# Optimization experiments

Hardware: AMD Instinct MI355X
Metric: run time of the kernel (lower is better)

The kernel has to match this reference:

```python
import jax, jax.numpy as jnp
import numpy as np

HID, OUT, D = 256, 64, 128
N_ITEM, N_USER, E = 100000, 50000, 800000


def sage_conv(x_src, x_dst, src, dst, w_l, b_l, w_r, n_dst):
    # PyG SAGEConv (mean aggr): out = lin_l(mean_j x_src[j]) + lin_r(x_dst)
    msg = x_src[src]                                        # [E, d_src] gather
    agg = jax.ops.segment_sum(msg, dst, num_segments=n_dst)  # [n_dst, d_src]
    cnt = jax.ops.segment_sum(jnp.ones((src.shape[0],), x_src.dtype), dst,
                              num_segments=n_dst)
    mean = agg / jnp.clip(cnt, 1.0, None)[:, None]
    return mean @ w_l + b_l + x_dst @ w_r


def setup_inputs() -> dict:
    key = jax.random.key(0)
    ks = jax.random.split(key, 16)
    sc = lambda d: 1.0 / np.sqrt(d)
    inp = {
        "x_item": jax.random.normal(ks[0], (N_ITEM, D), jnp.float32),
        "x_user": jax.random.normal(ks[1], (N_USER, D), jnp.float32),
        "ei_ii_src": jax.random.randint(ks[2], (E,), 0, N_ITEM),
        "ei_ii_dst": jax.random.randint(ks[3], (E,), 0, N_ITEM),
        "ei_iu_src": jax.random.randint(ks[4], (E,), 0, N_ITEM),
        "ei_iu_dst": jax.random.randint(ks[5], (E,), 0, N_USER),
        # conv1: item->item, in (D, D) -> HID
        "w_l1": jax.random.normal(ks[6], (D, HID), jnp.float32) * sc(D),
        "b1": jnp.zeros((HID,), jnp.float32),
        "w_r1": jax.random.normal(ks[7], (D, HID), jnp.float32) * sc(D),
        # conv2: (item D, user D) -> HID
        "w_l2": jax.random.normal(ks[8], (D, HID), jnp.float32) * sc(D),
        "b2": jnp.zeros((HID,), jnp.float32),
        "w_r2": jax.random.normal(ks[9], (D, HID), jnp.float32) * sc(D),
        # conv3: (item HID, user HID) -> HID
        "w_l3": jax.random.normal(ks[10], (HID, HID), jnp.float32) * sc(HID),
        "b3": jnp.zeros((HID,), jnp.float32),
        "w_r3": jax.random.normal(ks[11], (HID, HID), jnp.float32) * sc(HID),
        # final linear HID -> OUT
        "w_lin": jax.random.normal(ks[12], (HID, OUT), jnp.float32) * sc(HID),
        "b_lin": jnp.zeros((OUT,), jnp.float32),
    }
    return inp


def reference(x_item, x_user, ei_ii_src, ei_ii_dst, ei_iu_src, ei_iu_dst,
              w_l1, b1, w_r1, w_l2, b2, w_r2, w_l3, b3, w_r3, w_lin, b_lin):
    item_x = jax.nn.relu(sage_conv(x_item, x_item, ei_ii_src, ei_ii_dst,
                                   w_l1, b1, w_r1, N_ITEM))
    user_x = jax.nn.relu(sage_conv(x_item, x_user, ei_iu_src, ei_iu_dst,
                                   w_l2, b2, w_r2, N_USER))
    user_x = jax.nn.relu(sage_conv(item_x, user_x, ei_iu_src, ei_iu_dst,
                                   w_l3, b3, w_r3, N_USER))
    return user_x @ w_lin + b_lin
```

## Files before the change

kernel.cpp:

```cpp
#include <hip/hip_runtime.h>
#include <hip/hip_bf16.h>

#define N_ITEM 100000
#define N_USER 50000
#define D_IN   128
#define HID    256
#define OUT_D  64
#define CAP    64

#define S1B   391
#define CV1B  1024
#define CV2B  512
#define PK1B  68
#define G1 (S1B + CV1B + CV2B + PK1B)

#define S2B   391
#define A1B   3125
#define G2 (S2B + A1B)

#define C1B   782
#define A2B   1563
#define G3 (C1B + A2B)

#define C2B   391
#define A3LB  1568
#define G4 (C2B + A3LB)

#define C3LB  196
#define A3HB  1557
#define G5 (C3LB + A3HB)

#define C3HB  195
#define FLB   196
#define G6 (C3HB + FLB)

#define FHB   195

typedef __attribute__((ext_vector_type(8))) short bf16x8;
typedef __attribute__((ext_vector_type(4))) float f32x4;

__device__ inline float b2f(unsigned int h) {
    union { unsigned int u; float f; } c; c.u = h << 16; return c.f;
}
__device__ inline unsigned short f2b(float f) {
    unsigned int u = __builtin_bit_cast(unsigned int, f);
    u += 0x7fff + ((u >> 16) & 1);
    return (unsigned short)(u >> 16);
}

__device__ __forceinline__ void scatter_body(
    const int* __restrict__ src, const int* __restrict__ dstl,
    int* __restrict__ cur, int* __restrict__ slot, int E, int t)
{
    int e4 = t * 4;
    if (e4 + 3 < E) {
        int4 d = *(const int4*)&dstl[e4];
        int4 s = *(const int4*)&src[e4];
        int p0 = atomicAdd(&cur[d.x], 1);
        int p1 = atomicAdd(&cur[d.y], 1);
        int p2 = atomicAdd(&cur[d.z], 1);
        int p3 = atomicAdd(&cur[d.w], 1);
        if (p0 < CAP) slot[d.x * CAP + p0] = s.x;
        if (p1 < CAP) slot[d.y * CAP + p1] = s.y;
        if (p2 < CAP) slot[d.z * CAP + p2] = s.z;
        if (p3 < CAP) slot[d.w * CAP + p3] = s.w;
    } else {
        for (int e = e4; e < E; ++e) {
            int d0 = dstl[e], s0 = src[e];
            int p = atomicAdd(&cur[d0], 1);
            if (p < CAP) slot[d0 * CAP + p] = s0;
        }
    }
}

__device__ __forceinline__ void agg_mean128_q(
    const unsigned short* __restrict__ xsrc,
    const int* __restrict__ sl, int num, int ql,
    unsigned short* __restrict__ dstrow)
{
    const unsigned short* xb = xsrc + ql * 8;
    float acc[8] = {};
    int j = 0;
    for (; j + 8 <= num; j += 8) {
        int s[8];
        #pragma unroll
        for (int u = 0; u < 8; ++u) s[u] = sl[j + u];
        uint4 v[8];
        #pragma unroll
        for (int u = 0; u < 8; ++u)
            v[u] = *(const uint4*)(xb + (size_t)s[u] * 256);
        #pragma unroll
        for (int u = 0; u < 8; ++u) {
            acc[0] += b2f(v[u].x & 0xffffu);
            acc[1] += b2f(v[u].x >> 16);
            acc[2] += b2f(v[u].y & 0xffffu);
            acc[3] += b2f(v[u].y >> 16);
            acc[4] += b2f(v[u].z & 0xffffu);
            acc[5] += b2f(v[u].z >> 16);
            acc[6] += b2f(v[u].w & 0xffffu);
            acc[7] += b2f(v[u].w >> 16);
        }
    }
    for (; j < num; ++j) {
        uint4 v = *(const uint4*)(xb + (size_t)sl[j] * 256);
        acc[0] += b2f(v.x & 0xffffu);
        acc[1] += b2f(v.x >> 16);
        acc[2] += b2f(v.y & 0xffffu);
        acc[3] += b2f(v.y >> 16);
        acc[4] += b2f(v.z & 0xffffu);
        acc[5] += b2f(v.z >> 16);
        acc[6] += b2f(v.w & 0xffffu);
        acc[7] += b2f(v.w >> 16);
    }
    float sc = 1.0f / fmaxf((float)num, 1.0f);
    uint4 w;
    w.x = (unsigned int)f2b(acc[0] * sc) | ((unsigned int)f2b(acc[1] * sc) << 16);
    w.y = (unsigned int)f2b(acc[2] * sc) | ((unsigned int)f2b(acc[3] * sc) << 16);
    w.z = (unsigned int)f2b(acc[4] * sc) | ((unsigned int)f2b(acc[5] * sc) << 16);
    w.w = (unsigned int)f2b(acc[6] * sc) | ((unsigned int)f2b(acc[7] * sc) << 16);
    *(uint4*)(dstrow + ql * 8) = w;
}

__device__ __forceinline__ void agg_mean256_body(
    const unsigned short* __restrict__ xsrc,
    const int* __restrict__ sl, int num, int hl,
    unsigned short* __restrict__ dstrow)
{
    const unsigned short* xb = xsrc + hl * 8;
    float acc[8] = {};
    int j = 0;
    for (; j + 8 <= num; j += 8) {
        int s[8];
        #pragma unroll
        for (int u = 0; u < 8; ++u) s[u] = sl[j + u];
        uint4 v[8];
        #pragma unroll
        for (int u = 0; u < 8; ++u)
            v[u] = *(const uint4*)(xb + (size_t)s[u] * 256);
        #pragma unroll
        for (int u = 0; u < 8; ++u) {
            acc[0] += b2f(v[u].x & 0xffffu);
            acc[1] += b2f(v[u].x >> 16);
            acc[2] += b2f(v[u].y & 0xffffu);
            acc[3] += b2f(v[u].y >> 16);
            acc[4] += b2f(v[u].z & 0xffffu);
            acc[5] += b2f(v[u].z >> 16);
            acc[6] += b2f(v[u].w & 0xffffu);
            acc[7] += b2f(v[u].w >> 16);
        }
    }
    for (; j < num; ++j) {
        uint4 v = *(const uint4*)(xb + (size_t)sl[j] * 256);
        acc[0] += b2f(v.x & 0xffffu);
        acc[1] += b2f(v.x >> 16);
        acc[2] += b2f(v.y & 0xffffu);
        acc[3] += b2f(v.y >> 16);
        acc[4] += b2f(v.z & 0xffffu);
        acc[5] += b2f(v.z >> 16);
        acc[6] += b2f(v.w & 0xffffu);
        acc[7] += b2f(v.w >> 16);
    }
    float sc = 1.0f / fmaxf((float)num, 1.0f);
    uint4 w;
    w.x = (unsigned int)f2b(acc[0] * sc) | ((unsigned int)f2b(acc[1] * sc) << 16);
    w.y = (unsigned int)f2b(acc[2] * sc) | ((unsigned int)f2b(acc[3] * sc) << 16);
    w.z = (unsigned int)f2b(acc[4] * sc) | ((unsigned int)f2b(acc[5] * sc) << 16);
    w.w = (unsigned int)f2b(acc[6] * sc) | ((unsigned int)f2b(acc[7] * sc) << 16);
    *(uint4*)(dstrow + hl * 8) = w;
}

__device__ inline void pack_unit(const float* __restrict__ wl,
                                 const float* __restrict__ wr,
                                 int K, int NCv, unsigned short* __restrict__ dst,
                                 int u)
{
    int kb = u / NCv, col = u - kb * NCv;
    int colp = col ^ (kb & 7);
    unsigned short tmp[8];
    #pragma unroll
    for (int j = 0; j < 8; ++j) {
        int k = kb * 8 + j;
        float w = (k < K) ? wl[(size_t)k * NCv + col]
                          : wr[(size_t)(k - K) * NCv + col];
        tmp[j] = f2b(w);
    }
    *(uint4*)&dst[((size_t)kb * NCv + colp) * 8] = *(const uint4*)tmp;
}

__global__ __launch_bounds__(512) void prep1_kernel(
    const int* __restrict__ ii_src, const int* __restrict__ ii_dst,
    int* __restrict__ cur_i, int* __restrict__ slot_ii, int E,
    const float* __restrict__ x_item, const float* __restrict__ x_user,
    unsigned short* __restrict__ Acat1, unsigned short* __restrict__ Acat2,
    const float* __restrict__ wl1, const float* __restrict__ wr1,
    const float* __restrict__ wl2, const float* __restrict__ wr2,
    const float* __restrict__ wl3, const float* __restrict__ wr3,
    const float* __restrict__ wlin,
    unsigned short* __restrict__ Wp1, unsigned short* __restrict__ Wp2,
    unsigned short* __restrict__ Wp3, unsigned short* __restrict__ Wpl)
{
    int b = blockIdx.x;
    if (b < S1B) {
        scatter_body(ii_src, ii_dst, cur_i, slot_ii, E, b * 512 + threadIdx.x);
    } else if (b < S1B + CV1B) {
        const int STR = CV1B * 512;
        for (int u = (b - S1B) * 512 + threadIdx.x; u < N_ITEM * 32; u += STR) {
            int row = u >> 5, c4 = (u & 31) * 4;
            float4 v = *(const float4*)&x_item[(size_t)row * 128 + c4];
            ushort4 o;
            o.x = f2b(v.x); o.y = f2b(v.y); o.z = f2b(v.z); o.w = f2b(v.w);
            *(ushort4*)&Acat1[(size_t)row * 256 + 128 + c4] = o;
        }
    } else if (b < S1B + CV1B + CV2B) {
        const int STR = CV2B * 512;
        for (int u = (b - S1B - CV1B) * 512 + threadIdx.x; u < N_USER * 32; u += STR) {
            int row = u >> 5, c4 = (u & 31) * 4;
            float4 v = *(const float4*)&x_user[(size_t)row * 128 + c4];
            ushort4 o;
            o.x = f2b(v.x); o.y = f2b(v.y); o.z = f2b(v.z); o.w = f2b(v.w);
            *(ushort4*)&Acat2[(size_t)row * 256 + 128 + c4] = o;
        }
    } else {
        int t = (b - S1B - CV1B - CV2B) * 512 + threadIdx.x;
        if (t < 8192)       pack_unit(wl1, wr1, 128, 256, Wp1, t);
        else if (t < 16384) pack_unit(wl2, wr2, 128, 256, Wp2, t - 8192);
        else if (t < 32768) pack_unit(wl3, wr3, 256, 256, Wp3, t - 16384);
        else if (t < 34816) pack_unit(wlin, wlin, 256, 64, Wpl, t - 32768);
    }
}

__global__ __launch_bounds__(512) void prep2_kernel(
    const int* __restrict__ iu_src, const int* __restrict__ iu_dst,
    int* __restrict__ cur_u, int* __restrict__ slot_iu, int E,
    const unsigned short* __restrict__ xsrc,
    const int* __restrict__ slot_ii, const int* __restrict__ cur_i,
    unsigned short* __restrict__ Acat1)
{
    int b = blockIdx.x;
    if (b < S2B) {
        scatter_body(iu_src, iu_dst, cur_u, slot_iu, E, b * 512 + threadIdx.x);
        return;
    }
    int row = (b - S2B) * 32 + (threadIdx.x >> 4);
    int ql = threadIdx.x & 15;
    const int* sl = slot_ii + (size_t)row * CAP;
    int num = min(cur_i[row], CAP);
    agg_mean128_q(xsrc, sl, num, ql, Acat1 + (size_t)row * 256);
}

template <int NC, int WM, int WN, bool OUT_BF16, bool RELU>
__device__ __forceinline__ void gemm_body(
    int bid,
    const unsigned short* __restrict__ A, int lda,
    const unsigned short* __restrict__ Wp,
    const float* __restrict__ bias,
    void* __restrict__ Cout, int ldc, int col_off,
    int nrows, int nkt)
{
    constexpr int BM = 128;
    constexpr int MR = WM / 16, NR = WN / 16;
    constexpr int NWC = NC / WN;
    __shared__ unsigned short As[BM * 64];
    __shared__ unsigned short Bs[64 * NC];

    const int tid  = threadIdx.x;
    const int wave = tid >> 6;
    const int lane = tid & 63;
    const int row0 = bid * BM;
    const int wr = wave / NWC;
    const int wc = wave % NWC;

    f32x4 acc[MR][NR];
    #pragma unroll
    for (int m = 0; m < MR; ++m)
        #pragma unroll
        for (int n = 0; n < NR; ++n)
            acc[m][n] = (f32x4){0.f, 0.f, 0.f, 0.f};

    for (int kt = 0; kt < nkt; ++kt) {
        #pragma unroll
        for (int c = 0; c < 2; ++c) {
            int i = wave * 2 + c;
            int rl = 8 * i + (lane >> 3);
            int kc = (lane & 7) ^ (lane >> 3);
            const unsigned short* g =
                A + (size_t)(row0 + rl) * lda + kt * 64 + kc * 8;
            __builtin_amdgcn_global_load_lds(
                (const __attribute__((address_space(1))) void*)g,
                (__attribute__((address_space(3))) void*)(As + i * 512), 16, 0, 0);
        }
        constexpr int BCALLS = (64 * NC * 2) / 1024;
        constexpr int PW = BCALLS / 8;
        #pragma unroll
        for (int c = 0; c < PW; ++c) {
            int j = wave * PW + c;
            const unsigned short* g =
                Wp + (size_t)kt * (8 * NC * 8) + (size_t)j * 512 + lane * 8;
            __builtin_amdgcn_global_load_lds(
                (const __attribute__((address_space(1))) void*)g,
                (__attribute__((address_space(3))) void*)(Bs + j * 512), 16, 0, 0);
        }
        __syncthreads();

        #pragma unroll
        for (int kk = 0; kk < 2; ++kk) {
            bf16x8 af[MR], bfr[NR];
            #pragma unroll
            for (int m = 0; m < MR; ++m) {
                int row = wr * WM + m * 16 + (lane & 15);
                int kc = ((kk * 4) + (lane >> 4)) ^ (lane & 7);
                af[m] = *(const bf16x8*)(As + row * 64 + kc * 8);
            }
            #pragma unroll
            for (int n = 0; n < NR; ++n) {
                int kb = kk * 4 + (lane >> 4);
                int col = (wc * WN + n * 16 + (lane & 15)) ^ (kb & 7);
                bfr[n] = *(const bf16x8*)(Bs + (kb * NC + col) * 8);
            }
            #pragma unroll
            for (int m = 0; m < MR; ++m)
                #pragma unroll
                for (int n = 0; n < NR; ++n)
                    acc[m][n] = __builtin_amdgcn_mfma_f32_16x16x32_bf16(
                        af[m], bfr[n], acc[m][n], 0, 0, 0);
        }
        __syncthreads();
    }

    #pragma unroll
    for (int n = 0; n < NR; ++n) {
        int col = wc * WN + n * 16 + (lane & 15);
        float bv = bias[col];
        #pragma unroll
        for (int m = 0; m < MR; ++m) {
            #pragma unroll
            for (int j = 0; j < 4; ++j) {
                int row = row0 + wr * WM + m * 16 + (lane >> 4) * 4 + j;
                if (row < nrows) {
                    float v = acc[m][n][j] + bv;
                    if (RELU) v = fmaxf(v, 0.f);
                    if (OUT_BF16)
                        ((unsigned short*)Cout)[(size_t)row * ldc + col_off + col] = f2b(v);
                    else
                        ((float*)Cout)[(size_t)row * ldc + col_off + col] = v;
                }
            }
        }
    }
}

template <int NC, int WM, int WN, bool OUT_BF16, bool RELU>
__global__ __launch_bounds__(512) void gemm_mfma(
    int bid_base,
    const unsigned short* __restrict__ A, int lda,
    const unsigned short* __restrict__ Wp,
    const float* __restrict__ bias,
    void* __restrict__ Cout, int ldc, int col_off,
    int nrows, int nkt)
{
    gemm_body<NC, WM, WN, OUT_BF16, RELU>(bid_base + blockIdx.x, A, lda, Wp,
                                          bias, Cout, ldc, col_off, nrows, nkt);
}

__global__ __launch_bounds__(512) void conv1_agg2_kernel(
    const unsigned short* __restrict__ Acat1,
    const unsigned short* __restrict__ Wp1,
    const float* __restrict__ b1,
    unsigned short* __restrict__ item_x,
    const unsigned short* __restrict__ xsrc,
    const int* __restrict__ slot_iu, const int* __restrict__ cur_u,
    unsigned short* __restrict__ Acat2)
{
    if (blockIdx.x < C1B) {
        gemm_body<256, 64, 64, true, true>(blockIdx.x, Acat1, 256, Wp1, b1,
                                           item_x, 256, 0, N_ITEM, 4);
        return;
    }
    int row = (blockIdx.x - C1B) * 32 + (threadIdx.x >> 4);
    if (row >= N_USER) return;
    int ql = threadIdx.x & 15;
    const int* sl = slot_iu + (size_t)row * CAP;
    int num = min(cur_u[row], CAP);
    agg_mean128_q(xsrc, sl, num, ql, Acat2 + (size_t)row * 256);
}

__global__ __launch_bounds__(512) void conv2_agg3_kernel(
    const unsigned short* __restrict__ Acat2,
    const unsigned short* __restrict__ Wp2,
    const float* __restrict__ b2,
    unsigned short* __restrict__ Acat3,
    const unsigned short* __restrict__ item_x,
    const int* __restrict__ slot_iu, const int* __restrict__ cur_u)
{
    if (blockIdx.x < C2B) {
        gemm_body<256, 64, 64, true, true>(blockIdx.x, Acat2, 256, Wp2, b2,
                                           Acat3, 512, 256, N_USER, 4);
        return;
    }
    int row = (blockIdx.x - C2B) * 16 + (threadIdx.x >> 5);
    int hl = threadIdx.x & 31;
    const int* sl = slot_iu + (size_t)row * CAP;
    int num = min(cur_u[row], CAP);
    agg_mean256_body(item_x, sl, num, hl, Acat3 + (size_t)row * 512);
}

__global__ __launch_bounds__(512) void conv3_agg3b_kernel(
    const unsigned short* __restrict__ Acat3r,
    unsigned short* __restrict__ Acat3w,
    const unsigned short* __restrict__ Wp3,
    const float* __restrict__ b3,
    unsigned short* __restrict__ ux3,
    const unsigned short* __restrict__ item_x,
    const int* __restrict__ slot_iu, const int* __restrict__ cur_u)
{
    if (blockIdx.x < C3LB) {
        gemm_body<256, 64, 64, true, true>(blockIdx.x, Acat3r, 512, Wp3, b3,
                                           ux3, 256, 0, N_USER, 8);
        return;
    }
    int row = 25088 + (blockIdx.x - C3LB) * 16 + (threadIdx.x >> 5);
    int hl = threadIdx.x & 31;
    const int* sl = slot_iu + (size_t)row * CAP;
    int num = min(cur_u[row], CAP);
    agg_mean256_body(item_x, sl, num, hl, Acat3w + (size_t)row * 512);
}

__global__ __launch_bounds__(512) void conv3b_final_kernel(
    const unsigned short* __restrict__ Acat3,
    const unsigned short* __restrict__ Wp3,
    const float* __restrict__ b3,
    unsigned short* __restrict__ ux3,
    const unsigned short* __restrict__ Wpl,
    const float* __restrict__ b_lin,
    float* __restrict__ out)
{
    if (blockIdx.x < C3HB) {
        gemm_body<256, 64, 64, true, true>(C3LB + blockIdx.x, Acat3, 512, Wp3,
                                           b3, ux3, 256, 0, N_USER, 8);
    } else {
        gemm_body<64, 16, 64, false, false>(blockIdx.x - C3HB, ux3, 256, Wpl,
                                            b_lin, out, 64, 0, N_USER, 4);
    }
}

extern "C" void kernel_launch(void* const* d_in, const int* in_sizes, int n_in,
                              void* d_out, int out_size, void* d_ws, size_t ws_size,
                              hipStream_t stream)
{
    const float* x_item = (const float*)d_in[0];
    const float* x_user = (const float*)d_in[1];
    const int* ii_src   = (const int*)d_in[2];
    const int* ii_dst   = (const int*)d_in[3];
    const int* iu_src   = (const int*)d_in[4];
    const int* iu_dst   = (const int*)d_in[5];
    const float* w_l1 = (const float*)d_in[6];
    const float* b1   = (const float*)d_in[7];
    const float* w_r1 = (const float*)d_in[8];
    const float* w_l2 = (const float*)d_in[9];
    const float* b2   = (const float*)d_in[10];
    const float* w_r2 = (const float*)d_in[11];
    const float* w_l3 = (const float*)d_in[12];
    const float* b3   = (const float*)d_in[13];
    const float* w_r3 = (const float*)d_in[14];
    const float* w_lin = (const float*)d_in[15];
    const float* b_lin = (const float*)d_in[16];
    float* out = (float*)d_out;

    const int E = in_sizes[2];
    const int NIP = 100096;
    const int NUP = 50048;

    int* cur_i   = (int*)d_ws;
    int* cur_u   = cur_i + 100352;
    int* slot_ii = cur_u + 50176;
    int* slot_iu = slot_ii + (size_t)N_ITEM * CAP;

    unsigned short* Acat1  = (unsigned short*)(slot_iu + (size_t)N_USER * CAP);
    unsigned short* item_x = Acat1  + (size_t)NIP * 256;
    unsigned short* Acat2  = item_x + (size_t)NIP * 256;
    unsigned short* Acat3  = Acat2  + (size_t)NUP * 256;
    unsigned short* ux3    = Acat3  + (size_t)NUP * 512;
    unsigned short* Wp1    = ux3    + (size_t)NUP * 256;
    unsigned short* Wp2    = Wp1 + 65536;
    unsigned short* Wp3    = Wp2 + 65536;
    unsigned short* Wpl    = Wp3 + 131072;

    hipMemsetAsync(cur_i, 0, (size_t)150528 * 4, stream);

    prep1_kernel<<<G1, 512, 0, stream>>>(
        ii_src, ii_dst, cur_i, slot_ii, E,
        x_item, x_user, Acat1, Acat2,
        w_l1, w_r1, w_l2, w_r2, w_l3, w_r3, w_lin,
        Wp1, Wp2, Wp3, Wpl);

    prep2_kernel<<<G2, 512, 0, stream>>>(
        iu_src, iu_dst, cur_u, slot_iu, E,
        Acat1 + 128, slot_ii, cur_i, Acat1);

    conv1_agg2_kernel<<<G3, 512, 0, stream>>>(
        Acat1, Wp1, b1, item_x,
        Acat1 + 128, slot_iu, cur_u, Acat2);

    conv2_agg3_kernel<<<G4, 512, 0, stream>>>(
        Acat2, Wp2, b2, Acat3, item_x, slot_iu, cur_u);

    conv3_agg3b_kernel<<<G5, 512, 0, stream>>>(
        Acat3, Acat3, Wp3, b3, ux3, item_x, slot_iu, cur_u);

    conv3b_final_kernel<<<G6, 512, 0, stream>>>(
        Acat3, Wp3, b3, ux3, Wpl, b_lin, out);

    gemm_mfma<64, 16, 64, false, false><<<FHB, 512, 0, stream>>>(
        FLB, ux3, 256, Wpl, b_lin, out, 64, 0, N_USER, 4);
}
```

Measured before the change: 370.2 us.

## Replace staggered conv3/final overlap kernels with full agg then plain GEMMs

Removes the split scheme where conv3's GEMM and the final linear layer were run in halves alongside the remaining aggregation work across three launches. Conv2_agg3 now aggregates all user rows in one pass, followed by two plain GEMM launches for conv3 and the final projection. This simplifies the schedule and drops one launch, but gives up the overlap of GEMM work with the memory-bound aggregation. Launch counts use NUP/128, whose definition is not shown.

After: 365.2 us. About the same (-1.3%).

```diff
diff --git a/kernel.cpp b/kernel.cpp
--- a/kernel.cpp
+++ b/kernel.cpp
@@ -23,18 +23,8 @@
 #define G3 (C1B + A2B)
 
 #define C2B   391
-#define A3LB  1568
-#define G4 (C2B + A3LB)
-
-#define C3LB  196
-#define A3HB  1557
-#define G5 (C3LB + A3HB)
-
-#define C3HB  195
-#define FLB   196
-#define G6 (C3HB + FLB)
-
-#define FHB   195
+#define A3B   3125
+#define G4 (C2B + A3B)
 
 typedef __attribute__((ext_vector_type(8))) short bf16x8;
 typedef __attribute__((ext_vector_type(4))) float f32x4;
@@ -351,14 +341,13 @@
 
 template <int NC, int WM, int WN, bool OUT_BF16, bool RELU>
 __global__ __launch_bounds__(512) void gemm_mfma(
-    int bid_base,
     const unsigned short* __restrict__ A, int lda,
     const unsigned short* __restrict__ Wp,
     const float* __restrict__ bias,
     void* __restrict__ Cout, int ldc, int col_off,
     int nrows, int nkt)
 {
-    gemm_body<NC, WM, WN, OUT_BF16, RELU>(bid_base + blockIdx.x, A, lda, Wp,
+    gemm_body<NC, WM, WN, OUT_BF16, RELU>(blockIdx.x, A, lda, Wp,
                                           bias, Cout, ldc, col_off, nrows, nkt);
 }
 
@@ -402,45 +391,6 @@
     const int* sl = slot_iu + (size_t)row * CAP;
     int num = min(cur_u[row], CAP);
     agg_mean256_body(item_x, sl, num, hl, Acat3 + (size_t)row * 512);
-}
-
-__global__ __launch_bounds__(512) void conv3_agg3b_kernel(
-    const unsigned short* __restrict__ Acat3r,
-    unsigned short* __restrict__ Acat3w,
-    const unsigned short* __restrict__ Wp3,
-    const float* __restrict__ b3,
-    unsigned short* __restrict__ ux3,
-    const unsigned short* __restrict__ item_x,
-    const int* __restrict__ slot_iu, const int* __restrict__ cur_u)
-{
-    if (blockIdx.x < C3LB) {
-        gemm_body<256, 64, 64, true, true>(blockIdx.x, Acat3r, 512, Wp3, b3,
-                                           ux3, 256, 0, N_USER, 8);
-        return;
-    }
-    int row = 25088 + (blockIdx.x - C3LB) * 16 + (threadIdx.x >> 5);
-    int hl = threadIdx.x & 31;
-    const int* sl = slot_iu + (size_t)row * CAP;
-    int num = min(cur_u[row], CAP);
-    agg_mean256_body(item_x, sl, num, hl, Acat3w + (size_t)row * 512);
-}
-
-__global__ __launch_bounds__(512) void conv3b_final_kernel(
-    const unsigned short* __restrict__ Acat3,
-    const unsigned short* __restrict__ Wp3,
-    const float* __restrict__ b3,
-    unsigned short* __restrict__ ux3,
-    const unsigned short* __restrict__ Wpl,
-    const float* __restrict__ b_lin,
-    float* __restrict__ out)
-{
-    if (blockIdx.x < C3HB) {
-        gemm_body<256, 64, 64, true, true>(C3LB + blockIdx.x, Acat3, 512, Wp3,
-                                           b3, ux3, 256, 0, N_USER, 8);
-    } else {
-        gemm_body<64, 16, 64, false, false>(blockIdx.x - C3HB, ux3, 256, Wpl,
-                                            b_lin, out, 64, 0, N_USER, 4);
-    }
 }
 
 extern "C" void kernel_launch(void* const* d_in, const int* in_sizes, int n_in,
@@ -504,12 +454,9 @@
     conv2_agg3_kernel<<<G4, 512, 0, stream>>>(
         Acat2, Wp2, b2, Acat3, item_x, slot_iu, cur_u);
 
-    conv3_agg3b_kernel<<<G5, 512, 0, stream>>>(
-        Acat3, Acat3, Wp3, b3, ux3, item_x, slot_iu, cur_u);
-
-    conv3b_final_kernel<<<G6, 512, 0, stream>>>(
-        Acat3, Wp3, b3, ux3, Wpl, b_lin, out);
-
-    gemm_mfma<64, 16, 64, false, false><<<FHB, 512, 0, stream>>>(
-        FLB, ux3, 256, Wpl, b_lin, out, 64, 0, N_USER, 4);
-}
+    gemm_mfma<256, 64, 64, true, true><<<NUP / 128, 512, 0, stream>>>(
+        Acat3, 512, Wp3, b3, ux3, 256, 0, N_USER, 8);
+
+    gemm_mfma<64, 16, 64, false, false><<<NUP / 128, 512, 0, stream>>>(
+        ux3, 256, Wpl, b_lin, out, 64, 0, N_USER, 4);
+}
```
